# Optimization experiments

Measured on AMD Instinct MI355X. Metric: run time of the kernel, lower is better.

The kernel has to match this reference:

```python
import jax, jax.numpy as jnp
import numpy as np

DIM = 384
HEADS = 12
HEAD_DIM = DIM // HEADS
WIN = (2, 7, 7)
NW_TOK = WIN[0] * WIN[1] * WIN[2]  # 98
SCALE = HEAD_DIM ** -0.5


def _relative_position_index():
    d = np.arange(WIN[0]); h = np.arange(WIN[1]); w = np.arange(WIN[2])
    coords = np.stack(np.meshgrid(d, h, w, indexing='ij'))  # [3,D,H,W]
    cf = coords.reshape(3, -1)  # [3, NW_TOK]
    rel = cf[:, :, None] - cf[:, None, :]  # [3, N, N]
    rel = rel.transpose(1, 2, 0).astype(np.int64)
    rel[:, :, 0] += WIN[0] - 1
    rel[:, :, 1] += WIN[1] - 1
    rel[:, :, 2] += WIN[2] - 1
    rel[:, :, 0] *= (2 * WIN[1] - 1) * (2 * WIN[2] - 1)
    rel[:, :, 1] *= 2 * WIN[2] - 1
    return rel.sum(-1)  # [NW_TOK, NW_TOK]


def setup_inputs() -> dict:
    key = jax.random.key(0)
    ks = jax.random.split(key, 6)
    B_, N = 1024, NW_TOK + 1
    nW = 64
    table_len = (2 * WIN[0] - 1) * (2 * WIN[1] - 1) * (2 * WIN[2] - 1)  # 507
    x = jax.random.normal(ks[0], (B_, N, DIM), dtype=jnp.float32)
    mask = jax.random.normal(ks[1], (nW, NW_TOK, NW_TOK), dtype=jnp.float32)
    W_qkv = jax.random.normal(ks[2], (DIM, 3 * DIM), dtype=jnp.float32) * 0.02
    rpb_table = jax.random.normal(ks[3], (table_len, HEADS), dtype=jnp.float32) * 0.02
    W_proj = jax.random.normal(ks[4], (DIM, DIM), dtype=jnp.float32) * 0.02
    b_proj = jnp.zeros((DIM,), dtype=jnp.float32)
    rpi = jnp.asarray(_relative_position_index(), dtype=jnp.int32)
    return {"x": x, "mask": mask, "W_qkv": W_qkv, "rpb_table": rpb_table,
            "W_proj": W_proj, "b_proj": b_proj, "rpi": rpi}


def reference(x, mask, W_qkv, rpb_table, W_proj, b_proj, rpi):
    B_, N, C = x.shape
    qkv = (x @ W_qkv).reshape(B_, N, 3, HEADS, HEAD_DIM)
    q, k, v = qkv[:, :, 0], qkv[:, :, 1], qkv[:, :, 2]  # [B_, N, H, hd]
    attn = jnp.einsum('bnhd,bmhd->bhnm', q * SCALE, k)  # [B_, H, N, N]
    # gathered relative position bias over non-class tokens, zero-padded for class token
    bias = rpb_table[rpi.reshape(-1)].reshape(NW_TOK, NW_TOK, HEADS).transpose(2, 0, 1)
    bias_full = jnp.pad(bias, ((0, 0), (1, 0), (1, 0)))  # [H, N, N]
    attn = attn + bias_full[None]
    nW = mask.shape[0]
    mask_full = jnp.pad(mask, ((0, 0), (1, 0), (1, 0)))  # [nW, N, N]
    attn = attn.reshape(B_ // nW, nW, HEADS, N, N) + mask_full[None, :, None]
    attn = attn.reshape(B_, HEADS, N, N)
    attn = jax.nn.softmax(attn, axis=-1)
    out = jnp.einsum('bhnm,bmhd->bnhd', attn, v).reshape(B_, N, C)
    out = out @ W_proj + b_proj
    return out[:, 1:], out[:, :1]
```

## Files before the change

### kernel.cpp

```cpp
#include <hip/hip_runtime.h>
#include <hip/hip_bf16.h>
#include <cstddef>
#include <cstdint>


using bf16 = __hip_bfloat16;
typedef short v8s __attribute__((ext_vector_type(8)));
typedef float v4f __attribute__((ext_vector_type(4)));

static constexpr int    NTOK   = 99;
static constexpr int    CDIM   = 384;
static constexpr int    NHEAD  = 12;
static constexpr int    NROWS  = 101376;
static constexpr size_t PLANE  = (size_t)NROWS * 32;
static constexpr float  SCALEF = 0.17677669529663687f;

__device__ __forceinline__ v4f mfma16x16x32(v8s a, v8s b, v4f c) {
  return __builtin_amdgcn_mfma_f32_16x16x32_bf16(a, b, c, 0, 0, 0);
}
__device__ __forceinline__ short f2bf(float f) {
  bf16 h = __float2bfloat16(f);
  return *reinterpret_cast<short*>(&h);
}

static constexpr size_t WT_QKV_OFF = 0;
static constexpr size_t WT_P_OFF   = 884736;
static constexpr size_t BIAS_OFF   = 884736 + 294912;
static constexpr size_t COMMON_END = 1650096;
static constexpr size_t O_WS_OFF   = COMMON_END;
static constexpr size_t WS_MID     = O_WS_OFF + (size_t)NROWS * 384 * 2;
static constexpr size_t BM_OFF     = COMMON_END;
static constexpr size_t QKV_OFF    = BM_OFF + (size_t)64 * NHEAD * NTOK * NTOK * 4;
static constexpr size_t WS_FULL    = QKV_OFF + (size_t)NROWS * 1152 * 2;

static constexpr int PREP_BASE = 1152 * 384 + 384 * 384 + NHEAD * 99 * 99;
static constexpr int PREP_BM   = 64 * NHEAD * 99 * 99;

__global__ void prep_kernel(const float* __restrict__ Wqkv, const float* __restrict__ Wproj,
                            const float* __restrict__ rpb,  const int* __restrict__ rpi,
                            const float* __restrict__ mask,
                            bf16* __restrict__ WtQKV, bf16* __restrict__ WtP,
                            float* __restrict__ BIAS, float* __restrict__ BM, int do_bm)
{
  int idx = blockIdx.x * 256 + threadIdx.x;
  if (idx < 1152 * 384) {
    int c = idx / 384, k = idx - c * 384;
    WtQKV[idx] = __float2bfloat16(Wqkv[k * 1152 + c]);
  } else if (idx < 1152 * 384 + 384 * 384) {
    int j = idx - 1152 * 384;
    int c = j / 384, k = j - c * 384;
    WtP[j] = __float2bfloat16(Wproj[k * 384 + c]);
  } else if (idx < PREP_BASE) {
    int j = idx - (1152 * 384 + 384 * 384);
    int h = j / (99 * 99), r = j - h * (99 * 99);
    int nn = r / 99, mm = r - nn * 99;
    float v = 0.f;
    if (nn > 0 && mm > 0) v = rpb[rpi[(nn - 1) * 98 + (mm - 1)] * NHEAD + h];
    BIAS[j] = v;
  } else if (do_bm && idx < PREP_BASE + PREP_BM) {
    int j = idx - PREP_BASE;
    int wi = j / (NHEAD * 9801);
    int r2 = j - wi * (NHEAD * 9801);
    int h = r2 / 9801, rr = r2 - h * 9801;
    int nn = rr / 99, mm = rr - nn * 99;
    float v = 0.f;
    if (nn > 0 && mm > 0)
      v = rpb[rpi[(nn - 1) * 98 + (mm - 1)] * NHEAD + h]
        + mask[((size_t)wi * 98 + (nn - 1)) * 98 + (mm - 1)];
    BM[j] = v;
  }
}

static constexpr int GQ_LD    = 72;
static constexpr int GQ_OFFB  = 0;
static constexpr int GQ_OFFA  = 192 * GQ_LD * 2;
static constexpr int GQ_LDS   = GQ_OFFA + 128 * GQ_LD * 2;
static constexpr int CSTG_LD  = 104;

__global__ __launch_bounds__(512)
void k_qkv(const float* __restrict__ x, const bf16* __restrict__ WtQKV,
           bf16* __restrict__ qkv2)
{
  __shared__ __align__(16) char smem[GQ_LDS];
  bf16* B_lds = (bf16*)(smem + GQ_OFFB);
  bf16* A_lds = (bf16*)(smem + GQ_OFFA);
  bf16* C_stg = (bf16*)(smem);

  const int tid  = threadIdx.x;
  const int wave = tid >> 6;
  const int wm   = wave >> 2;
  const int wn   = wave & 3;
  const int lane = tid & 63;
  const int g    = lane >> 4;
  const int li   = lane & 15;
  const int tile = (blockIdx.x & 7) * 594 + (blockIdx.x >> 3);
  const int R0   = (tile / 6) * 128;
  const int CN   = (tile % 6) * 192;

  v4f acc[4][3];
  #pragma unroll
  for (int mi = 0; mi < 4; ++mi)
    #pragma unroll
    for (int ni = 0; ni < 3; ++ni) acc[mi][ni] = (v4f){0.f, 0.f, 0.f, 0.f};

  for (int kc = 0; kc < 6; ++kc) {
    const int k0 = kc * 64;
    #pragma unroll
    for (int p = 0; p < 3; ++p) {
      int it = tid + p * 512, rr = it >> 3, k8 = it & 7;
      *(v8s*)(B_lds + rr * GQ_LD + k8 * 8) =
          *(const v8s*)(WtQKV + (size_t)(CN + rr) * 384 + k0 + k8 * 8);
    }
    #pragma unroll
    for (int p = 0; p < 2; ++p) {
      int it = tid + p * 512, rr = it >> 3, k8 = it & 7;
      const float* src = x + (size_t)(R0 + rr) * 384 + k0 + k8 * 8;
      v4f x0 = *(const v4f*)(src);
      v4f x1 = *(const v4f*)(src + 4);
      v8s f;
      #pragma unroll
      for (int j = 0; j < 4; ++j) { f[j] = f2bf(x0[j]); f[j + 4] = f2bf(x1[j]); }
      *(v8s*)(A_lds + rr * GQ_LD + k8 * 8) = f;
    }
    __syncthreads();
    #pragma unroll
    for (int ks = 0; ks < 2; ++ks) {
      v8s af[4], bfr[3];
      #pragma unroll
      for (int mi = 0; mi < 4; ++mi)
        af[mi] = *(const v8s*)(A_lds + (wm * 64 + mi * 16 + li) * GQ_LD + ks * 32 + g * 8);
      #pragma unroll
      for (int ni = 0; ni < 3; ++ni)
        bfr[ni] = *(const v8s*)(B_lds + (wn * 48 + ni * 16 + li) * GQ_LD + ks * 32 + g * 8);
      #pragma unroll
      for (int mi = 0; mi < 4; ++mi)
        #pragma unroll
        for (int ni = 0; ni < 3; ++ni)
          acc[mi][ni] = mfma16x16x32(af[mi], bfr[ni], acc[mi][ni]);
    }
    __syncthreads();
  }

  const float scale = (CN < 384) ? SCALEF : 1.f;
  const int r_ep = tid >> 2, d8 = tid & 3;
  #pragma unroll
  for (int half = 0; half < 2; ++half) {
    __syncthreads();
    if ((wn >> 1) == half) {
      #pragma unroll
      for (int mi = 0; mi < 4; ++mi)
        #pragma unroll
        for (int ni = 0; ni < 3; ++ni)
          #pragma unroll
          for (int j = 0; j < 4; ++j)
            C_stg[(wm * 64 + mi * 16 + g * 4 + j) * CSTG_LD + (wn & 1) * 48 + ni * 16 + li] =
                __float2bfloat16(acc[mi][ni][j] * scale);
    }
    __syncthreads();
    #pragma unroll
    for (int cidx = 0; cidx < 3; ++cidx) {
      int c_global = CN + half * 96 + cidx * 32;
      int seg = c_global / 384, hh = (c_global % 384) >> 5;
      bf16* plane = qkv2 + (size_t)(hh * 3 + seg) * PLANE;
      v8s val = *(const v8s*)(C_stg + r_ep * CSTG_LD + cidx * 32 + d8 * 8);
      *(v8s*)(plane + (size_t)(R0 + r_ep) * 32 + d8 * 8) = val;
    }
  }
}

static constexpr int A_QK_LD = 40;
static constexpr int A_VT_LD = 104;
static constexpr int A_P_LD  = 104;
static constexpr int A_OFF_Q = 0;
static constexpr int A_OFF_K = A_OFF_Q + 112 * A_QK_LD * 2;
static constexpr int A_OFF_V = A_OFF_K + 112 * A_QK_LD * 2;
static constexpr int A_OFF_P = A_OFF_V + 32  * A_VT_LD * 2;
static constexpr int A_LDS   = A_OFF_P + 112 * A_P_LD  * 2;

__global__ __launch_bounds__(448)
void k_attn(const float* __restrict__ BM, bf16* __restrict__ qkv2)
{
  __shared__ __align__(16) char smem[A_LDS];
  bf16* q_lds  = (bf16*)(smem + A_OFF_Q);
  bf16* k_lds  = (bf16*)(smem + A_OFF_K);
  bf16* vT_lds = (bf16*)(smem + A_OFF_V);
  bf16* P_lds  = (bf16*)(smem + A_OFF_P);

  const int b    = blockIdx.x;
  const int h0   = blockIdx.y * 6;
  const int tid  = threadIdx.x;
  const int wave = tid >> 6;
  const int lane = tid & 63;
  const int g    = lane >> 4;
  const int li   = lane & 15;
  const int wi   = b & 63;

  const int r  = tid >> 2, l4 = tid & 3;
  const int rc = (r > 98) ? 98 : r;
  const size_t goff = ((size_t)b * NTOK + rc) * 32 + l4 * 8;

  {
    v8s pq = *(const v8s*)(qkv2 + (size_t)(h0 * 3 + 0) * PLANE + goff);
    v8s pk = *(const v8s*)(qkv2 + (size_t)(h0 * 3 + 1) * PLANE + goff);
    v8s pv = *(const v8s*)(qkv2 + (size_t)(h0 * 3 + 2) * PLANE + goff);
    *(v8s*)(q_lds + r * A_QK_LD + l4 * 8) = pq;
    *(v8s*)(k_lds + r * A_QK_LD + l4 * 8) = pk;
    if (r < NTOK) {
      #pragma unroll
      for (int e = 0; e < 8; ++e)
        *(short*)(vT_lds + (l4 * 8 + e) * A_VT_LD + r) = pv[e];
    }
  }
  __syncthreads();

  for (int hi = 0; hi < 6; ++hi) {
    const int h = h0 + hi;
    v8s nq, nk, nv;
    if (hi < 5) {
      nq = *(const v8s*)(qkv2 + (size_t)(h * 3 + 3) * PLANE + goff);
      nk = *(const v8s*)(qkv2 + (size_t)(h * 3 + 4) * PLANE + goff);
      nv = *(const v8s*)(qkv2 + (size_t)(h * 3 + 5) * PLANE + goff);
    }

    const float* bm = BM + (size_t)(wi * NHEAD + h) * 9801;
    float bmr[28];
    #pragma unroll
    for (int t = 0; t < 7; ++t) {
      int col = 16 * t + li; int colc = (col > 98) ? 98 : col;
      #pragma unroll
      for (int j = 0; j < 4; ++j) {
        int row = 16 * wave + g * 4 + j; int rowc = (row > 98) ? 98 : row;
        bmr[t * 4 + j] = bm[rowc * 99 + colc];
      }
    }

    v8s aq = *(const v8s*)(q_lds + (16 * wave + li) * A_QK_LD + g * 8);
    v4f sacc[7];
    #pragma unroll
    for (int t = 0; t < 7; ++t) {
      v8s bk = *(const v8s*)(k_lds + (16 * t + li) * A_QK_LD + g * 8);
      v4f z = (v4f){0.f, 0.f, 0.f, 0.f};
      sacc[t] = mfma16x16x32(aq, bk, z);
    }
    #pragma unroll
    for (int t = 0; t < 7; ++t) {
      int col = 16 * t + li;
      #pragma unroll
      for (int j = 0; j < 4; ++j) {
        float s = sacc[t][j];
        if (col >= NTOK) s = -1e30f;
        else             s += bmr[t * 4 + j];
        sacc[t][j] = s;
      }
    }
    float linv[4];
    #pragma unroll
    for (int j = 0; j < 4; ++j) {
      float m = -1e30f;
      #pragma unroll
      for (int t = 0; t < 7; ++t) m = fmaxf(m, sacc[t][j]);
      m = fmaxf(m, __shfl_xor(m, 1));
      m = fmaxf(m, __shfl_xor(m, 2));
      m = fmaxf(m, __shfl_xor(m, 4));
      m = fmaxf(m, __shfl_xor(m, 8));
      float l = 0.f;
      #pragma unroll
      for (int t = 0; t < 7; ++t) {
        float p = __expf(sacc[t][j] - m);
        sacc[t][j] = p;
        l += p;
      }
      l += __shfl_xor(l, 1);
      l += __shfl_xor(l, 2);
      l += __shfl_xor(l, 4);
      l += __shfl_xor(l, 8);
      linv[j] = 1.f / l;
      int row = 16 * wave + g * 4 + j;
      #pragma unroll
      for (int t = 0; t < 7; ++t) {
        int col = 16 * t + li;
        if (col < NTOK) P_lds[row * A_P_LD + col] = __float2bfloat16(sacc[t][j]);
      }
    }
    v4f oacc[2];
    oacc[0] = (v4f){0.f, 0.f, 0.f, 0.f};
    oacc[1] = (v4f){0.f, 0.f, 0.f, 0.f};
    #pragma unroll
    for (int ks = 0; ks < 3; ++ks) {
      v8s ap = *(const v8s*)(P_lds + (16 * wave + li) * A_P_LD + ks * 32 + g * 8);
      #pragma unroll
      for (int t = 0; t < 2; ++t) {
        v8s bv = *(const v8s*)(vT_lds + (16 * t + li) * A_VT_LD + ks * 32 + g * 8);
        oacc[t] = mfma16x16x32(ap, bv, oacc[t]);
      }
    }
    #pragma unroll
    for (int t = 0; t < 2; ++t) {
      float v0 = __bfloat162float(vT_lds[(16 * t + li) * A_VT_LD + 96]);
      float v1 = __bfloat162float(vT_lds[(16 * t + li) * A_VT_LD + 97]);
      float v2 = __bfloat162float(vT_lds[(16 * t + li) * A_VT_LD + 98]);
      #pragma unroll
      for (int j = 0; j < 4; ++j) {
        int row = 16 * wave + g * 4 + j;
        float p0 = __bfloat162float(P_lds[row * A_P_LD + 96]);
        float p1 = __bfloat162float(P_lds[row * A_P_LD + 97]);
        float p2 = __bfloat162float(P_lds[row * A_P_LD + 98]);
        oacc[t][j] += p0 * v0 + p1 * v1 + p2 * v2;
      }
    }
    bf16* oplane = qkv2 + (size_t)(h * 3) * PLANE;
    #pragma unroll
    for (int t = 0; t < 2; ++t) {
      #pragma unroll
      for (int j = 0; j < 4; ++j) {
        int row = 16 * wave + g * 4 + j;
        if (row < NTOK)
          oplane[((size_t)b * NTOK + row) * 32 + 16 * t + li] =
              __float2bfloat16(oacc[t][j] * linv[j]);
      }
    }
    __syncthreads();
    if (hi < 5) {
      *(v8s*)(q_lds + r * A_QK_LD + l4 * 8) = nq;
      *(v8s*)(k_lds + r * A_QK_LD + l4 * 8) = nk;
      if (r < NTOK) {
        #pragma unroll
        for (int e = 0; e < 8; ++e)
          *(short*)(vT_lds + (l4 * 8 + e) * A_VT_LD + r) = nv[e];
      }
      __syncthreads();
    }
  }
}

static constexpr int K2_LD   = 72;
static constexpr int K2_OFFW = 0;
static constexpr int K2_OFFO = 192 * K2_LD * 2;
static constexpr int K2_LDS  = K2_OFFO + 128 * K2_LD * 2;

__global__ __launch_bounds__(512)
void k2_proj(const bf16* __restrict__ O_src, const int hm,
             const bf16* __restrict__ WtP, const float* __restrict__ bproj,
             float* __restrict__ out)
{
  __shared__ __align__(16) char smem[K2_LDS];
  bf16* W_lds = (bf16*)(smem + K2_OFFW);
  bf16* O_lds = (bf16*)(smem + K2_OFFO);

  const int tid  = threadIdx.x;
  const int wave = tid >> 6;
  const int wm   = wave >> 2;
  const int wn   = wave & 3;
  const int lane = tid & 63;
  const int g    = lane >> 4;
  const int li   = lane & 15;
  const int tile = (blockIdx.x & 7) * 198 + (blockIdx.x >> 3);
  const int R0   = (tile >> 1) * 128;
  const int CN   = (tile & 1) * 192;

  v4f acc[4][3];
  #pragma unroll
  for (int mi = 0; mi < 4; ++mi)
    #pragma unroll
    for (int ni = 0; ni < 3; ++ni) acc[mi][ni] = (v4f){0.f, 0.f, 0.f, 0.f};

  for (int kc = 0; kc < 6; ++kc) {
    const int k0 = kc * 64;
    #pragma unroll
    for (int p = 0; p < 3; ++p) {
      int it = tid + p * 512, rr = it >> 3, k8 = it & 7;
      *(v8s*)(W_lds + rr * K2_LD + k8 * 8) =
          *(const v8s*)(WtP + (size_t)(CN + rr) * CDIM + k0 + k8 * 8);
    }
    #pragma unroll
    for (int p = 0; p < 2; ++p) {
      int it = tid + p * 512, rr = it >> 3, k8 = it & 7;
      const bf16* src;
      if (hm) {
        int c = k0 + k8 * 8, hh = c >> 5, d = c & 31;
        src = O_src + (size_t)(hh * 3) * PLANE + (size_t)(R0 + rr) * 32 + d;
      } else {
        src = O_src + (size_t)(R0 + rr) * 384 + k0 + k8 * 8;
      }
      *(v8s*)(O_lds + rr * K2_LD + k8 * 8) = *(const v8s*)src;
    }
    __syncthreads();
    #pragma unroll
    for (int ks = 0; ks < 2; ++ks) {
      v8s af[4], bfr[3];
      #pragma unroll
      for (int mi = 0; mi < 4; ++mi)
        af[mi] = *(const v8s*)(O_lds + (wm * 64 + mi * 16 + li) * K2_LD + ks * 32 + g * 8);
      #pragma unroll
      for (int ni = 0; ni < 3; ++ni)
        bfr[ni] = *(const v8s*)(W_lds + (wn * 48 + ni * 16 + li) * K2_LD + ks * 32 + g * 8);
      #pragma unroll
      for (int mi = 0; mi < 4; ++mi)
        #pragma unroll
        for (int ni = 0; ni < 3; ++ni)
          acc[mi][ni] = mfma16x16x32(af[mi], bfr[ni], acc[mi][ni]);
    }
    __syncthreads();
  }

  const size_t OUT2 = (size_t)1024 * 98 * CDIM;
  #pragma unroll
  for (int mi = 0; mi < 4; ++mi)
    #pragma unroll
    for (int ni = 0; ni < 3; ++ni) {
      int col = CN + wn * 48 + ni * 16 + li;
      float bb = bproj[col];
      #pragma unroll
      for (int j = 0; j < 4; ++j) {
        int rr = R0 + wm * 64 + mi * 16 + g * 4 + j;
        int b = rr / 99, n = rr - b * 99;
        float v = acc[mi][ni][j] + bb;
        if (n == 0) out[OUT2 + (size_t)b * CDIM + col] = v;
        else        out[((size_t)b * 98 + (n - 1)) * CDIM + col] = v;
      }
    }
}

static constexpr int QK_LD = 40;
static constexpr int VT_LD = 136;
static constexpr int P_LD  = 136;
static constexpr int WS_LD = 104;
static constexpr int K1_OFF_Q = 0;
static constexpr int K1_OFF_K = K1_OFF_Q + 112 * QK_LD * 2;
static constexpr int K1_OFF_V = K1_OFF_K + 112 * QK_LD * 2;
static constexpr int K1_OFF_P = K1_OFF_V + 32  * VT_LD * 2;
static constexpr int K1_OFF_W = K1_OFF_P + 112 * P_LD  * 2;
static constexpr int K1_LDS   = K1_OFF_W + 96 * WS_LD * 2;

__global__ __launch_bounds__(512)
void k1_attn(const float* __restrict__ x, const float* __restrict__ mask,
             const float* __restrict__ BIAS, const bf16* __restrict__ WtQKV,
             bf16* __restrict__ O_ws)
{
  __shared__ __align__(16) char smem[K1_LDS];
  bf16* q_lds  = (bf16*)(smem + K1_OFF_Q);
  bf16* k_lds  = (bf16*)(smem + K1_OFF_K);
  bf16* vT_lds = (bf16*)(smem + K1_OFF_V);
  bf16* P_lds  = (bf16*)(smem + K1_OFF_P);
  bf16* w_lds  = (bf16*)(smem + K1_OFF_W);

  const int b    = blockIdx.x;
  const int tid  = threadIdx.x;
  const int wave = tid >> 6;
  const int lane = tid & 63;
  const int g    = lane >> 4;
  const int li   = lane & 15;
  const int wi   = b & 63;

  v8s afr[12];
  if (wave < 7) {
    int arow = 16 * wave + li; if (arow > 98) arow = 98;
    const float* xb = x + ((size_t)b * NTOK + arow) * CDIM + g * 8;
    #pragma unroll
    for (int s = 0; s < 12; ++s) {
      v4f x0 = *(const v4f*)(xb + s * 32);
      v4f x1 = *(const v4f*)(xb + s * 32 + 4);
      v8s f;
      #pragma unroll
      for (int j = 0; j < 4; ++j) { f[j] = f2bf(x0[j]); f[j + 4] = f2bf(x1[j]); }
      afr[s] = f;
    }
  }

  for (int h = 0; h < NHEAD; ++h) {
    v4f qacc[6];
    #pragma unroll
    for (int t = 0; t < 6; ++t) qacc[t] = (v4f){0.f, 0.f, 0.f, 0.f};
    #pragma unroll
    for (int c4 = 0; c4 < 4; ++c4) {
      for (int idx = tid; idx < 96 * 12; idx += 512) {
        int rr = idx / 12, ch = idx - rr * 12;
        int cg = (rr < 32) ? (h * 32 + rr)
               : (rr < 64) ? (CDIM + h * 32 + rr - 32)
                           : (2 * CDIM + h * 32 + rr - 64);
        *(v8s*)(w_lds + rr * WS_LD + ch * 8) =
            *(const v8s*)(WtQKV + (size_t)cg * CDIM + c4 * 96 + ch * 8);
      }
      __syncthreads();
      if (wave < 7) {
        #pragma unroll
        for (int ss = 0; ss < 3; ++ss) {
          const int s = c4 * 3 + ss;
          #pragma unroll
          for (int t = 0; t < 6; ++t) {
            v8s bw = *(const v8s*)(w_lds + (16 * t + li) * WS_LD + ss * 32 + g * 8);
            qacc[t] = mfma16x16x32(afr[s], bw, qacc[t]);
          }
        }
      }
      __syncthreads();
    }
    if (wave < 7) {
      #pragma unroll
      for (int t = 0; t < 6; ++t) {
        #pragma unroll
        for (int j = 0; j < 4; ++j) {
          int row = 16 * wave + g * 4 + j;
          int col = 16 * (t & 1) + li;
          float v = qacc[t][j];
          if (t < 2)      q_lds[row * QK_LD + col] = __float2bfloat16(v * SCALEF);
          else if (t < 4) k_lds[row * QK_LD + col] = __float2bfloat16(v);
          else            vT_lds[col * VT_LD + row] = __float2bfloat16(v);
        }
      }
    }
    vT_lds[(tid >> 4) * VT_LD + 112 + (tid & 15)] = __float2bfloat16(0.f);
    __syncthreads();

    if (wave < 7) {
      v8s aq = *(const v8s*)(q_lds + (16 * wave + li) * QK_LD + g * 8);
      v4f sacc[7];
      #pragma unroll
      for (int t = 0; t < 7; ++t) {
        v8s bk = *(const v8s*)(k_lds + (16 * t + li) * QK_LD + g * 8);
        v4f z = (v4f){0.f, 0.f, 0.f, 0.f};
        sacc[t] = mfma16x16x32(aq, bk, z);
      }
      #pragma unroll
      for (int t = 0; t < 7; ++t) {
        int col = 16 * t + li;
        #pragma unroll
        for (int j = 0; j < 4; ++j) {
          int row = 16 * wave + g * 4 + j;
          float s = sacc[t][j];
          if (col >= NTOK) s = -1e30f;
          else if (row < NTOK) {
            s += BIAS[(h * NTOK + row) * NTOK + col];
            if (row > 0 && col > 0)
              s += mask[((size_t)wi * 98 + (row - 1)) * 98 + (col - 1)];
          }
          sacc[t][j] = s;
        }
      }
      float linv[4];
      #pragma unroll
      for (int j = 0; j < 4; ++j) {
        float m = -1e30f;
        #pragma unroll
        for (int t = 0; t < 7; ++t) m = fmaxf(m, sacc[t][j]);
        m = fmaxf(m, __shfl_xor(m, 1));
        m = fmaxf(m, __shfl_xor(m, 2));
        m = fmaxf(m, __shfl_xor(m, 4));
        m = fmaxf(m, __shfl_xor(m, 8));
        float l = 0.f;
        #pragma unroll
        for (int t = 0; t < 7; ++t) {
          float p = __expf(sacc[t][j] - m);
          sacc[t][j] = p;
          l += p;
        }
        l += __shfl_xor(l, 1);
        l += __shfl_xor(l, 2);
        l += __shfl_xor(l, 4);
        l += __shfl_xor(l, 8);
        linv[j] = 1.f / l;
        int row = 16 * wave + g * 4 + j;
        #pragma unroll
        for (int t = 0; t < 7; ++t)
          P_lds[row * P_LD + 16 * t + li] = __float2bfloat16(sacc[t][j]);
        P_lds[row * P_LD + 112 + li] = __float2bfloat16(0.f);
      }
      v4f oacc[2];
      oacc[0] = (v4f){0.f, 0.f, 0.f, 0.f};
      oacc[1] = (v4f){0.f, 0.f, 0.f, 0.f};
      #pragma unroll
      for (int ks = 0; ks < 4; ++ks) {
        v8s ap = *(const v8s*)(P_lds + (16 * wave + li) * P_LD + ks * 32 + g * 8);
        #pragma unroll
        for (int t = 0; t < 2; ++t) {
          v8s bv = *(const v8s*)(vT_lds + (16 * t + li) * VT_LD + ks * 32 + g * 8);
          oacc[t] = mfma16x16x32(ap, bv, oacc[t]);
        }
      }
      #pragma unroll
      for (int t = 0; t < 2; ++t) {
        #pragma unroll
        for (int j = 0; j < 4; ++j) {
          int row = 16 * wave + g * 4 + j;
          if (row < NTOK)
            O_ws[((size_t)b * 99 + row) * CDIM + h * 32 + 16 * t + li] =
                __float2bfloat16(oacc[t][j] * linv[j]);
        }
      }
    }
    __syncthreads();
  }
}

static constexpr int M_O_LD = 392;
static constexpr int M_OFF_O = 0;
static constexpr int M_OFF_Q = M_OFF_O + 99  * M_O_LD * 2;
static constexpr int M_OFF_K = M_OFF_Q + 112 * QK_LD * 2;
static constexpr int M_OFF_V = M_OFF_K + 112 * QK_LD * 2;
static constexpr int M_OFF_P = M_OFF_V + 32  * VT_LD * 2;
static constexpr int M_OFF_W = M_OFF_P + 112 * P_LD  * 2;
static constexpr int M_LDS   = M_OFF_W + 96 * WS_LD * 2;

__global__ __launch_bounds__(512)
void fused_mono(const float* __restrict__ x, const float* __restrict__ mask,
                const float* __restrict__ bproj, const float* __restrict__ BIAS,
                const bf16* __restrict__ WtQKV, const bf16* __restrict__ WtP,
                float* __restrict__ out)
{
  __shared__ __align__(16) char smem[M_LDS];
  bf16* O_lds  = (bf16*)(smem + M_OFF_O);
  bf16* q_lds  = (bf16*)(smem + M_OFF_Q);
  bf16* k_lds  = (bf16*)(smem + M_OFF_K);
  bf16* vT_lds = (bf16*)(smem + M_OFF_V);
  bf16* P_lds  = (bf16*)(smem + M_OFF_P);
  bf16* w_lds  = (bf16*)(smem + M_OFF_W);

  const int b    = blockIdx.x;
  const int tid  = threadIdx.x;
  const int wave = tid >> 6;
  const int lane = tid & 63;
  const int g    = lane >> 4;
  const int li   = lane & 15;
  const int wi   = b & 63;

  v8s afr[12];
  if (wave < 7) {
    int arow = 16 * wave + li; if (arow > 98) arow = 98;
    const float* xb = x + ((size_t)b * NTOK + arow) * CDIM + g * 8;
    #pragma unroll
    for (int s = 0; s < 12; ++s) {
      v4f x0 = *(const v4f*)(xb + s * 32);
      v4f x1 = *(const v4f*)(xb + s * 32 + 4);
      v8s f;
      #pragma unroll
      for (int j = 0; j < 4; ++j) { f[j] = f2bf(x0[j]); f[j + 4] = f2bf(x1[j]); }
      afr[s] = f;
    }
  }

  for (int h = 0; h < NHEAD; ++h) {
    v4f qacc[6];
    #pragma unroll
    for (int t = 0; t < 6; ++t) qacc[t] = (v4f){0.f, 0.f, 0.f, 0.f};
    #pragma unroll
    for (int c4 = 0; c4 < 4; ++c4) {
      for (int idx = tid; idx < 96 * 12; idx += 512) {
        int rr = idx / 12, ch = idx - rr * 12;
        int cg = (rr < 32) ? (h * 32 + rr)
               : (rr < 64) ? (CDIM + h * 32 + rr - 32)
                           : (2 * CDIM + h * 32 + rr - 64);
        *(v8s*)(w_lds + rr * WS_LD + ch * 8) =
            *(const v8s*)(WtQKV + (size_t)cg * CDIM + c4 * 96 + ch * 8);
      }
      __syncthreads();
      if (wave < 7) {
        #pragma unroll
        for (int ss = 0; ss < 3; ++ss) {
          const int s = c4 * 3 + ss;
          #pragma unroll
          for (int t = 0; t < 6; ++t) {
            v8s bw = *(const v8s*)(w_lds + (16 * t + li) * WS_LD + ss * 32 + g * 8);
            qacc[t] = mfma16x16x32(afr[s], bw, qacc[t]);
          }
        }
      }
      __syncthreads();
    }
    if (wave < 7) {
      #pragma unroll
      for (int t = 0; t < 6; ++t) {
        #pragma unroll
        for (int j = 0; j < 4; ++j) {
          int row = 16 * wave + g * 4 + j;
          int col = 16 * (t & 1) + li;
          float v = qacc[t][j];
          if (t < 2)      q_lds[row * QK_LD + col] = __float2bfloat16(v * SCALEF);
          else if (t < 4) k_lds[row * QK_LD + col] = __float2bfloat16(v);
          else            vT_lds[col * VT_LD + row] = __float2bfloat16(v);
        }
      }
    }
    vT_lds[(tid >> 4) * VT_LD + 112 + (tid & 15)] = __float2bfloat16(0.f);
    __syncthreads();

    if (wave < 7) {
      v8s aq = *(const v8s*)(q_lds + (16 * wave + li) * QK_LD + g * 8);
      v4f sacc[7];
      #pragma unroll
      for (int t = 0; t < 7; ++t) {
        v8s bk = *(const v8s*)(k_lds + (16 * t + li) * QK_LD + g * 8);
        v4f z = (v4f){0.f, 0.f, 0.f, 0.f};
        sacc[t] = mfma16x16x32(aq, bk, z);
      }
      #pragma unroll
      for (int t = 0; t < 7; ++t) {
        int col = 16 * t + li;
        #pragma unroll
        for (int j = 0; j < 4; ++j) {
          int row = 16 * wave + g * 4 + j;
          float s = sacc[t][j];
          if (col >= NTOK) s = -1e30f;
          else if (row < NTOK) {
            s += BIAS[(h * NTOK + row) * NTOK + col];
            if (row > 0 && col > 0)
              s += mask[((size_t)wi * 98 + (row - 1)) * 98 + (col - 1)];
          }
          sacc[t][j] = s;
        }
      }
      float linv[4];
      #pragma unroll
      for (int j = 0; j < 4; ++j) {
        float m = -1e30f;
        #pragma unroll
        for (int t = 0; t < 7; ++t) m = fmaxf(m, sacc[t][j]);
        m = fmaxf(m, __shfl_xor(m, 1));
        m = fmaxf(m, __shfl_xor(m, 2));
        m = fmaxf(m, __shfl_xor(m, 4));
        m = fmaxf(m, __shfl_xor(m, 8));
        float l = 0.f;
        #pragma unroll
        for (int t = 0; t < 7; ++t) {
          float p = __expf(sacc[t][j] - m);
          sacc[t][j] = p;
          l += p;
        }
        l += __shfl_xor(l, 1);
        l += __shfl_xor(l, 2);
        l += __shfl_xor(l, 4);
        l += __shfl_xor(l, 8);
        linv[j] = 1.f / l;
        int row = 16 * wave + g * 4 + j;
        #pragma unroll
        for (int t = 0; t < 7; ++t)
          P_lds[row * P_LD + 16 * t + li] = __float2bfloat16(sacc[t][j]);
        P_lds[row * P_LD + 112 + li] = __float2bfloat16(0.f);
      }
      v4f oacc[2];
      oacc[0] = (v4f){0.f, 0.f, 0.f, 0.f};
      oacc[1] = (v4f){0.f, 0.f, 0.f, 0.f};
      #pragma unroll
      for (int ks = 0; ks < 4; ++ks) {
        v8s ap = *(const v8s*)(P_lds + (16 * wave + li) * P_LD + ks * 32 + g * 8);
        #pragma unroll
        for (int t = 0; t < 2; ++t) {
          v8s bv = *(const v8s*)(vT_lds + (16 * t + li) * VT_LD + ks * 32 + g * 8);
          oacc[t] = mfma16x16x32(ap, bv, oacc[t]);
        }
      }
      #pragma unroll
      for (int t = 0; t < 2; ++t) {
        #pragma unroll
        for (int j = 0; j < 4; ++j) {
          int row = 16 * wave + g * 4 + j;
          if (row < NTOK)
            O_lds[row * M_O_LD + h * 32 + 16 * t + li] =
                __float2bfloat16(oacc[t][j] * linv[j]);
        }
      }
    }
    __syncthreads();
  }

  const size_t OUT2 = (size_t)1024 * 98 * CDIM;
  const int orow_clamped = (16 * wave + li > 98) ? 98 : 16 * wave + li;
  for (int cc = 0; cc < 4; ++cc) {
    v4f pacc[6];
    #pragma unroll
    for (int t = 0; t < 6; ++t) pacc[t] = (v4f){0.f, 0.f, 0.f, 0.f};
    for (int c4 = 0; c4 < 4; ++c4) {
      for (int idx = tid; idx < 96 * 12; idx += 512) {
        int rr = idx / 12, ch = idx - rr * 12;
        *(v8s*)(w_lds + rr * WS_LD + ch * 8) =
            *(const v8s*)(WtP + ((size_t)(cc * 96 + rr)) * CDIM + c4 * 96 + ch * 8);
      }
      __syncthreads();
      if (wave < 7) {
        #pragma unroll
        for (int ss = 0; ss < 3; ++ss) {
          const int s = c4 * 3 + ss;
          v8s ao = *(const v8s*)(O_lds + orow_clamped * M_O_LD + s * 32 + g * 8);
          #pragma unroll
          for (int t = 0; t < 6; ++t) {
            v8s bw = *(const v8s*)(w_lds + (16 * t + li) * WS_LD + ss * 32 + g * 8);
            pacc[t] = mfma16x16x32(ao, bw, pacc[t]);
          }
        }
      }
      __syncthreads();
    }
    if (wave < 7) {
      #pragma unroll
      for (int t = 0; t < 6; ++t) {
        #pragma unroll
        for (int j = 0; j < 4; ++j) {
          int row = 16 * wave + g * 4 + j;
          if (row < NTOK) {
            int col = cc * 96 + 16 * t + li;
            float v = pacc[t][j] + bproj[col];
            if (row == 0) out[OUT2 + (size_t)b * CDIM + col] = v;
            else          out[((size_t)b * 98 + (row - 1)) * CDIM + col] = v;
          }
        }
      }
    }
  }
}

extern "C" void kernel_launch(void* const* d_in, const int* in_sizes, int n_in,
                              void* d_out, int out_size, void* d_ws, size_t ws_size,
                              hipStream_t stream) {
  const float* x     = (const float*)d_in[0];
  const float* mask  = (const float*)d_in[1];
  const float* Wqkv  = (const float*)d_in[2];
  const float* rpb   = (const float*)d_in[3];
  const float* Wproj = (const float*)d_in[4];
  const float* bproj = (const float*)d_in[5];
  const int*   rpi   = (const int*)d_in[6];

  bf16*  WtQKV = (bf16*)((char*)d_ws + WT_QKV_OFF);
  bf16*  WtP   = (bf16*)((char*)d_ws + WT_P_OFF);
  float* BIAS  = (float*)((char*)d_ws + BIAS_OFF);

  const bool full = (ws_size >= WS_FULL);
  const int prep_items = full ? (PREP_BASE + PREP_BM) : PREP_BASE;
  float* BM = (float*)((char*)d_ws + BM_OFF);
  prep_kernel<<<(prep_items + 255) / 256, 256, 0, stream>>>(
      Wqkv, Wproj, rpb, rpi, mask, WtQKV, WtP, BIAS, BM, full ? 1 : 0);

  if (full) {
    bf16* qkv2 = (bf16*)((char*)d_ws + QKV_OFF);
    k_qkv<<<792 * 6, 512, 0, stream>>>(x, WtQKV, qkv2);
    k_attn<<<dim3(1024, 2), 448, 0, stream>>>(BM, qkv2);
    k2_proj<<<792 * 2, 512, 0, stream>>>(qkv2, 1, WtP, bproj, (float*)d_out);
  } else if (ws_size >= WS_MID) {
    bf16* O_ws = (bf16*)((char*)d_ws + O_WS_OFF);
    k1_attn<<<1024, 512, 0, stream>>>(x, mask, BIAS, WtQKV, O_ws);
    k2_proj<<<792 * 2, 512, 0, stream>>>(O_ws, 0, WtP, bproj, (float*)d_out);
  } else {
    fused_mono<<<1024, 512, 0, stream>>>(x, mask, bproj, BIAS, WtQKV, WtP,
                                         (float*)d_out);
  }
}
```

Baseline: 425.7 us.

## Register-prefetch QKV GEMM tiles and load attention Q/K fragments directly from global

The QKV projection GEMM now prefetches the next K-chunk of weights and x into registers while MFMAs run on the current LDS tile, then converts and writes to LDS after a barrier. The goal is to overlap global load latency with compute. The attention kernel drops the Q and K LDS staging and loads MFMA fragments straight from global memory each head, keeping only V transposed in LDS. This reduces LDS traffic and footprint, but issues more redundant global/L2 reads, since every wave reloads all seven K fragments, and raises register pressure.

```diff
diff --git a/kernel.cpp b/kernel.cpp
--- a/kernel.cpp
+++ b/kernel.cpp
@@ -97,32 +97,49 @@
   const int R0   = (tile / 6) * 128;
   const int CN   = (tile % 6) * 192;
 
+  const int brr = tid >> 3, bk8 = tid & 7;
+  const int arr = tid >> 3, ak8 = tid & 7;
+
   v4f acc[4][3];
   #pragma unroll
   for (int mi = 0; mi < 4; ++mi)
     #pragma unroll
     for (int ni = 0; ni < 3; ++ni) acc[mi][ni] = (v4f){0.f, 0.f, 0.f, 0.f};
 
+  v8s breg[3];
+  v4f areg[2][2];
+
+  auto load_regs = [&](int kc) {
+    const int k0 = kc * 64;
+    #pragma unroll
+    for (int p = 0; p < 3; ++p)
+      breg[p] = *(const v8s*)(WtQKV + (size_t)(CN + brr + p * 64) * 384 + k0 + bk8 * 8);
+    #pragma unroll
+    for (int p = 0; p < 2; ++p) {
+      const float* src = x + (size_t)(R0 + arr + p * 64) * 384 + k0 + ak8 * 8;
+      areg[p][0] = *(const v4f*)(src);
+      areg[p][1] = *(const v4f*)(src + 4);
+    }
+  };
+  auto write_lds = [&]() {
+    #pragma unroll
+    for (int p = 0; p < 3; ++p)
+      *(v8s*)(B_lds + (brr + p * 64) * GQ_LD + bk8 * 8) = breg[p];
+    #pragma unroll
+    for (int p = 0; p < 2; ++p) {
+      v8s f;
+      #pragma unroll
+      for (int j = 0; j < 4; ++j) { f[j] = f2bf(areg[p][0][j]); f[j + 4] = f2bf(areg[p][1][j]); }
+      *(v8s*)(A_lds + (arr + p * 64) * GQ_LD + ak8 * 8) = f;
+    }
+  };
+
+  load_regs(0);
+  write_lds();
+  __syncthreads();
+
   for (int kc = 0; kc < 6; ++kc) {
-    const int k0 = kc * 64;
-    #pragma unroll
-    for (int p = 0; p < 3; ++p) {
-      int it = tid + p * 512, rr = it >> 3, k8 = it & 7;
-      *(v8s*)(B_lds + rr * GQ_LD + k8 * 8) =
-          *(const v8s*)(WtQKV + (size_t)(CN + rr) * 384 + k0 + k8 * 8);
-    }
-    #pragma unroll
-    for (int p = 0; p < 2; ++p) {
-      int it = tid + p * 512, rr = it >> 3, k8 = it & 7;
-      const float* src = x + (size_t)(R0 + rr) * 384 + k0 + k8 * 8;
-      v4f x0 = *(const v4f*)(src);
-      v4f x1 = *(const v4f*)(src + 4);
-      v8s f;
-      #pragma unroll
-      for (int j = 0; j < 4; ++j) { f[j] = f2bf(x0[j]); f[j + 4] = f2bf(x1[j]); }
-      *(v8s*)(A_lds + rr * GQ_LD + k8 * 8) = f;
-    }
-    __syncthreads();
+    if (kc < 5) load_regs(kc + 1);
     #pragma unroll
     for (int ks = 0; ks < 2; ++ks) {
       v8s af[4], bfr[3];
@@ -139,6 +156,10 @@
           acc[mi][ni] = mfma16x16x32(af[mi], bfr[ni], acc[mi][ni]);
     }
     __syncthreads();
+    if (kc < 5) {
+      write_lds();
+      __syncthreads();
+    }
   }
 
   const float scale = (CN < 384) ? SCALEF : 1.f;
@@ -168,21 +189,16 @@
   }
 }
 
-static constexpr int A_QK_LD = 40;
 static constexpr int A_VT_LD = 104;
 static constexpr int A_P_LD  = 104;
-static constexpr int A_OFF_Q = 0;
-static constexpr int A_OFF_K = A_OFF_Q + 112 * A_QK_LD * 2;
-static constexpr int A_OFF_V = A_OFF_K + 112 * A_QK_LD * 2;
-static constexpr int A_OFF_P = A_OFF_V + 32  * A_VT_LD * 2;
-static constexpr int A_LDS   = A_OFF_P + 112 * A_P_LD  * 2;
+static constexpr int A_OFF_V = 0;
+static constexpr int A_OFF_P = A_OFF_V + 32 * A_VT_LD * 2;
+static constexpr int A_LDS   = A_OFF_P + 112 * A_P_LD * 2;
 
 __global__ __launch_bounds__(448)
 void k_attn(const float* __restrict__ BM, bf16* __restrict__ qkv2)
 {
   __shared__ __align__(16) char smem[A_LDS];
-  bf16* q_lds  = (bf16*)(smem + A_OFF_Q);
-  bf16* k_lds  = (bf16*)(smem + A_OFF_K);
   bf16* vT_lds = (bf16*)(smem + A_OFF_V);
   bf16* P_lds  = (bf16*)(smem + A_OFF_P);
 
@@ -195,16 +211,20 @@
   const int li   = lane & 15;
   const int wi   = b & 63;
 
-  const int r  = tid >> 2, l4 = tid & 3;
-  const int rc = (r > 98) ? 98 : r;
-  const size_t goff = ((size_t)b * NTOK + rc) * 32 + l4 * 8;
+  const int r = tid >> 2, l4 = tid & 3;
+  const size_t voff = ((size_t)b * NTOK + ((r > 98) ? 98 : r)) * 32 + l4 * 8;
+
+  const int qrow = (16 * wave + li > 98) ? 98 : 16 * wave + li;
+  const size_t qoff = ((size_t)b * NTOK + qrow) * 32 + g * 8;
+  size_t koff[7];
+  #pragma unroll
+  for (int t = 0; t < 7; ++t) {
+    int krow = 16 * t + li; if (krow > 98) krow = 98;
+    koff[t] = ((size_t)b * NTOK + krow) * 32 + g * 8;
+  }
 
   {
-    v8s pq = *(const v8s*)(qkv2 + (size_t)(h0 * 3 + 0) * PLANE + goff);
-    v8s pk = *(const v8s*)(qkv2 + (size_t)(h0 * 3 + 1) * PLANE + goff);
-    v8s pv = *(const v8s*)(qkv2 + (size_t)(h0 * 3 + 2) * PLANE + goff);
-    *(v8s*)(q_lds + r * A_QK_LD + l4 * 8) = pq;
-    *(v8s*)(k_lds + r * A_QK_LD + l4 * 8) = pk;
+    v8s pv = *(const v8s*)(qkv2 + (size_t)(h0 * 3 + 2) * PLANE + voff);
     if (r < NTOK) {
       #pragma unroll
       for (int e = 0; e < 8; ++e)
@@ -215,12 +235,14 @@
 
   for (int hi = 0; hi < 6; ++hi) {
     const int h = h0 + hi;
-    v8s nq, nk, nv;
-    if (hi < 5) {
-      nq = *(const v8s*)(qkv2 + (size_t)(h * 3 + 3) * PLANE + goff);
-      nk = *(const v8s*)(qkv2 + (size_t)(h * 3 + 4) * PLANE + goff);
-      nv = *(const v8s*)(qkv2 + (size_t)(h * 3 + 5) * PLANE + goff);
-    }
+    v8s nv;
+    if (hi < 5) nv = *(const v8s*)(qkv2 + (size_t)(h * 3 + 5) * PLANE + voff);
+
+    const bf16* kp = qkv2 + (size_t)(h * 3 + 1) * PLANE;
+    v8s kf[7];
+    #pragma unroll
+    for (int t = 0; t < 7; ++t) kf[t] = *(const v8s*)(kp + koff[t]);
+    v8s qf = *(const v8s*)(qkv2 + (size_t)(h * 3 + 0) * PLANE + qoff);
 
     const float* bm = BM + (size_t)(wi * NHEAD + h) * 9801;
     float bmr[28];
@@ -234,13 +256,11 @@
       }
     }
 
-    v8s aq = *(const v8s*)(q_lds + (16 * wave + li) * A_QK_LD + g * 8);
     v4f sacc[7];
     #pragma unroll
     for (int t = 0; t < 7; ++t) {
-      v8s bk = *(const v8s*)(k_lds + (16 * t + li) * A_QK_LD + g * 8);
       v4f z = (v4f){0.f, 0.f, 0.f, 0.f};
-      sacc[t] = mfma16x16x32(aq, bk, z);
+      sacc[t] = mfma16x16x32(qf, kf[t], z);
     }
     #pragma unroll
     for (int t = 0; t < 7; ++t) {
@@ -321,8 +341,6 @@
     }
     __syncthreads();
     if (hi < 5) {
-      *(v8s*)(q_lds + r * A_QK_LD + l4 * 8) = nq;
-      *(v8s*)(k_lds + r * A_QK_LD + l4 * 8) = nk;
       if (r < NTOK) {
         #pragma unroll
         for (int e = 0; e < 8; ++e)
```

Result: slower. 437.0 us (+2.6%).
